# Kernel tuning notes

Measured on AMD Instinct MI355X. Metric: run time of the kernel, lower is better.

The kernel has to match this reference:

```python
import jax, jax.numpy as jnp
import numpy as np

B, T, D = 4, 4096, 1024
H, HD, K = 16, 64, 32
TAU, THRESHOLD, PULSE_BASE, N_STEPS = 0.1, 0.5, 4.0, 5


def setup_inputs() -> dict:
    key = jax.random.key(0)
    ks = jax.random.split(key, 8)
    s = 0.02
    return {
        "x": jax.random.normal(ks[0], (B, T, D), jnp.float32),
        "spectral_basis": jax.random.normal(ks[1], (B, T, K), jnp.float32) / np.sqrt(T),
        "W_qkv": jax.random.normal(ks[2], (3 * D, D), jnp.float32) * s,
        "W_out": jax.random.normal(ks[3], (D, D), jnp.float32) * s,
        "a": jnp.float32(0.7),
        "b": jnp.float32(0.8),
        "W1": jax.random.normal(ks[4], (HD // 2, HD), jnp.float32) * s,
        "b1": jnp.zeros((HD // 2,), jnp.float32),
        "W2": jax.random.normal(ks[5], (1, HD // 2), jnp.float32) * s,
        "b2": jnp.zeros((1,), jnp.float32),
        "spectral_filter": jnp.full((H, 32), 0.5, jnp.float32),
    }


def soliton_dynamics(stimulus, a, b):
    # stimulus: (B, H, K, HD); FitzHugh-Nagumo style 5-step Euler integration
    dt = 1.0 / N_STEPS
    v = jnp.zeros_like(stimulus)
    w = jnp.zeros_like(stimulus)
    stim_scale = jnp.clip(jnp.max(jnp.abs(stimulus), axis=-1, keepdims=True), 1e-06, None)
    stim_n = stimulus / stim_scale
    I = jnp.where(jnp.abs(stimulus) > THRESHOLD, stim_n, stim_n * 0.1)
    for _ in range(N_STEPS):
        dv = v - v ** 3 / 3 - w + I
        dw = (v + a - b * w) / TAU
        v = jnp.clip(v + dt * dv, -3.0, 3.0)
        w = jnp.clip(w + dt * dw, -3.0, 3.0)
    return v * stim_scale, v


def reference(x, spectral_basis, W_qkv, W_out, a, b, W1, b1, W2, b2, spectral_filter):
    Bx, Tx, Dx = x.shape
    k = spectral_basis.shape[-1]
    qkv = x @ W_qkv.T                                   # (B,T,3D)
    qkv = qkv.reshape(Bx, Tx, 3, H, HD).transpose(2, 0, 3, 1, 4)
    q, kk, v = qkv[0], qkv[1], qkv[2]                   # (B,H,T,HD)

    qm = q.mean(axis=2)                                 # (B,H,HD)
    h1 = jax.nn.silu(qm @ W1.T + b1)
    pulse_widths = PULSE_BASE + jax.nn.softplus(h1 @ W2.T + b2)[..., 0]  # (B,H)

    q_spec = jnp.einsum('bhtd,btk->bhkd', q, spectral_basis)
    k_spec = jnp.einsum('bhtd,btk->bhkd', kk, spectral_basis)
    attn_spec = jnp.einsum('bhkd,bhkd->bhk', q_spec, k_spec) / np.sqrt(HD)
    filt = jax.nn.sigmoid(spectral_filter[:, :k])       # (H,k)
    attn_spec = attn_spec * filt[None]

    stim = jnp.broadcast_to(attn_spec[..., None], (Bx, H, k, HD))
    response, state = soliton_dynamics(stim, a, b)
    response = response.mean(axis=-1)                   # (B,H,k)

    v_spec = jnp.einsum('bhtd,btk->bhkd', v, spectral_basis)
    out_spec = response[..., None] * v_spec             # (B,H,k,HD)
    out = jnp.einsum('bhkd,btk->bhtd', out_spec, spectral_basis)
    out = out.transpose(0, 2, 1, 3).reshape(Bx, Tx, Dx)
    out = out @ W_out.T
    return out, pulse_widths, response
```

## Files before the change

kernel.cpp:

```cpp
#include <hip/hip_runtime.h>

#define B_ 4
#define T_ 4096
#define D_ 1024
#define H_ 16
#define K_ 32


__global__ __launch_bounds__(256) void reduce_zp(
    const float4* __restrict__ src, float4* __restrict__ dst,
    const int n4, const int z, const int stride4, const int total4)
{
  int i = blockIdx.x * 256 + threadIdx.x;
  if (i >= total4) return;
  if (i >= n4){
    float4 zv; zv.x = 0.f; zv.y = 0.f; zv.z = 0.f; zv.w = 0.f;
    dst[i] = zv; return;
  }
  float s0 = 0.f, s1 = 0.f, s2 = 0.f, s3 = 0.f;
  const float4* p = src + i;
  for (int zz = 0; zz < z; ++zz){
    float4 v = p[(size_t)zz * stride4];
    s0 += v.x; s1 += v.y; s2 += v.z; s3 += v.w;
  }
  float4 o; o.x = s0; o.y = s1; o.z = s2; o.w = s3;
  dst[i] = o;
}

__global__ __launch_bounds__(256) void reduce_z(
    const float4* __restrict__ src, float4* __restrict__ dst,
    const int n4, const int z, const int stride4)
{
  int i = blockIdx.x * 256 + threadIdx.x;
  if (i >= n4) return;
  float s0 = 0.f, s1 = 0.f, s2 = 0.f, s3 = 0.f;
  const float4* p = src + i;
  for (int zz = 0; zz < z; ++zz){
    float4 v = p[(size_t)zz * stride4];
    s0 += v.x; s1 += v.y; s2 += v.z; s3 += v.w;
  }
  float4 o; o.x = s0; o.y = s1; o.z = s2; o.w = s3;
  dst[i] = o;
}

__global__ __launch_bounds__(256) void k1_spectral_p(
    const float* __restrict__ x, const float* __restrict__ sb,
    float* __restrict__ XP)
{
  const int b  = blockIdx.y;
  const int zz = blockIdx.z;
  const int t0 = zz * 64;
  const int c  = blockIdx.x * 256 + threadIdx.x;
  __shared__ __align__(16) float sbs[64][36];
  #pragma unroll
  for (int i = 0; i < 8; i++){
    int idx = threadIdx.x + i * 256;
    int k = idx & 31, t = idx >> 5;
    sbs[t][k] = sb[(size_t)(b * T_ + t0 + t) * K_ + k];
  }
  __syncthreads();
  float acc[32];
  #pragma unroll
  for (int k = 0; k < 32; k++) acc[k] = 0.f;
  float am = 0.f;
  const float* xp = x + (size_t)(b * T_ + t0) * D_ + c;
  float p0 = xp[0];
  float p1 = xp[D_];
  float p2 = xp[2 * D_];
  float p3 = xp[3 * D_];
  #pragma unroll 4
  for (int t = 0; t < 64; ++t){
    float xv = p0; p0 = p1; p1 = p2; p2 = p3;
    if (t < 60) p3 = xp[(size_t)(t + 4) * D_];
    am += xv;
    const float4* srow = (const float4*)&sbs[t][0];
    #pragma unroll
    for (int j = 0; j < 8; j++){
      float4 s4 = srow[j];
      acc[j * 4 + 0] = fmaf(s4.x, xv, acc[j * 4 + 0]);
      acc[j * 4 + 1] = fmaf(s4.y, xv, acc[j * 4 + 1]);
      acc[j * 4 + 2] = fmaf(s4.z, xv, acc[j * 4 + 2]);
      acc[j * 4 + 3] = fmaf(s4.w, xv, acc[j * 4 + 3]);
    }
  }
  float* o = XP + (size_t)zz * 135168 + (size_t)(b * K_) * D_ + c;
  #pragma unroll
  for (int k = 0; k < 32; k++) o[(size_t)k * D_] = acc[k];
  XP[(size_t)zz * 135168 + 131072 + b * D_ + c] = am;
}

__global__ __launch_bounds__(256) void gemm_aw_p(
    const float* __restrict__ A, const float* __restrict__ W,
    float* __restrict__ Cp, const int N, const int cPerSplit, const int MN)
{
  __shared__ __align__(16) float As[32][68];
  __shared__ __align__(16) float Ws[32][68];
  const int nt = blockIdx.x, mt = blockIdx.y;
  const int cbase = blockIdx.z * cPerSplit;
  const int tx = threadIdx.x & 15, ty = threadIdx.x >> 4;
  const int sc = threadIdx.x & 31, sr = threadIdx.x >> 5;
  float acc[4][4];
  #pragma unroll
  for (int i = 0; i < 4; i++)
    #pragma unroll
    for (int j = 0; j < 4; j++) acc[i][j] = 0.f;

  float ra[8], rw[8];
  const float* Ap = A + (size_t)(mt * 64 + sr) * 1024 + cbase + sc;
  const float* Wp = W + (size_t)(nt * 64 + sr) * 1024 + cbase + sc;
  #pragma unroll
  for (int i = 0; i < 8; i++){ ra[i] = Ap[(size_t)(i * 8) * 1024];
                               rw[i] = Wp[(size_t)(i * 8) * 1024]; }
  #pragma unroll
  for (int i = 0; i < 8; i++){ As[sc][sr + i * 8] = ra[i];
                               Ws[sc][sr + i * 8] = rw[i]; }
  __syncthreads();

  for (int cc = 32; cc < cPerSplit; cc += 32){
    #pragma unroll
    for (int i = 0; i < 8; i++){ ra[i] = Ap[(size_t)(i * 8) * 1024 + cc];
                                 rw[i] = Wp[(size_t)(i * 8) * 1024 + cc]; }
    #pragma unroll 4
    for (int c = 0; c < 32; ++c){
      const float4 a4 = *(const float4*)&As[c][ty * 4];
      const float4 w4 = *(const float4*)&Ws[c][tx * 4];
      acc[0][0] = fmaf(a4.x, w4.x, acc[0][0]);
      acc[0][1] = fmaf(a4.x, w4.y, acc[0][1]);
      acc[0][2] = fmaf(a4.x, w4.z, acc[0][2]);
      acc[0][3] = fmaf(a4.x, w4.w, acc[0][3]);
      acc[1][0] = fmaf(a4.y, w4.x, acc[1][0]);
      acc[1][1] = fmaf(a4.y, w4.y, acc[1][1]);
      acc[1][2] = fmaf(a4.y, w4.z, acc[1][2]);
      acc[1][3] = fmaf(a4.y, w4.w, acc[1][3]);
      acc[2][0] = fmaf(a4.z, w4.x, acc[2][0]);
      acc[2][1] = fmaf(a4.z, w4.y, acc[2][1]);
      acc[2][2] = fmaf(a4.z, w4.z, acc[2][2]);
      acc[2][3] = fmaf(a4.z, w4.w, acc[2][3]);
      acc[3][0] = fmaf(a4.w, w4.x, acc[3][0]);
      acc[3][1] = fmaf(a4.w, w4.y, acc[3][1]);
      acc[3][2] = fmaf(a4.w, w4.z, acc[3][2]);
      acc[3][3] = fmaf(a4.w, w4.w, acc[3][3]);
    }
    __syncthreads();
    #pragma unroll
    for (int i = 0; i < 8; i++){ As[sc][sr + i * 8] = ra[i];
                                 Ws[sc][sr + i * 8] = rw[i]; }
    __syncthreads();
  }
  #pragma unroll 4
  for (int c = 0; c < 32; ++c){
    const float4 a4 = *(const float4*)&As[c][ty * 4];
    const float4 w4 = *(const float4*)&Ws[c][tx * 4];
    acc[0][0] = fmaf(a4.x, w4.x, acc[0][0]);
    acc[0][1] = fmaf(a4.x, w4.y, acc[0][1]);
    acc[0][2] = fmaf(a4.x, w4.z, acc[0][2]);
    acc[0][3] = fmaf(a4.x, w4.w, acc[0][3]);
    acc[1][0] = fmaf(a4.y, w4.x, acc[1][0]);
    acc[1][1] = fmaf(a4.y, w4.y, acc[1][1]);
    acc[1][2] = fmaf(a4.y, w4.z, acc[1][2]);
    acc[1][3] = fmaf(a4.y, w4.w, acc[1][3]);
    acc[2][0] = fmaf(a4.z, w4.x, acc[2][0]);
    acc[2][1] = fmaf(a4.z, w4.y, acc[2][1]);
    acc[2][2] = fmaf(a4.z, w4.z, acc[2][2]);
    acc[2][3] = fmaf(a4.z, w4.w, acc[2][3]);
    acc[3][0] = fmaf(a4.w, w4.x, acc[3][0]);
    acc[3][1] = fmaf(a4.w, w4.y, acc[3][1]);
    acc[3][2] = fmaf(a4.w, w4.z, acc[3][2]);
    acc[3][3] = fmaf(a4.w, w4.w, acc[3][3]);
  }
  float* cp = Cp + (size_t)blockIdx.z * MN;
  #pragma unroll
  for (int i = 0; i < 4; i++){
    float4 o; o.x = acc[i][0]; o.y = acc[i][1]; o.z = acc[i][2]; o.w = acc[i][3];
    *(float4*)(cp + (size_t)(mt * 64 + ty * 4 + i) * N + nt * 64 + tx * 4) = o;
  }
}

__global__ __launch_bounds__(64) void k3_small(
    const float* __restrict__ qkvC,
    const float* __restrict__ W1, const float* __restrict__ b1,
    const float* __restrict__ W2, const float* __restrict__ b2,
    const float* __restrict__ filt,
    const float* __restrict__ a_in, const float* __restrict__ b_in,
    float* __restrict__ u, float* __restrict__ out_pulse,
    float* __restrict__ out_resp)
{
  const int b = blockIdx.x >> 4, h = blockIdx.x & 15;
  const int d = threadIdx.x;
  __shared__ float qm[64];
  __shared__ float h1s[32];
  __shared__ float rsp[32];
  qm[d] = qkvC[(size_t)(128 + b) * 3072 + h * 64 + d] * (1.0f / 4096.0f);
  __syncthreads();
  if (d < 32){
    float z = b1[d];
    for (int j = 0; j < 64; j++) z = fmaf(qm[j], W1[d * 64 + j], z);
    h1s[d] = z / (1.0f + __expf(-z));
  }
  __syncthreads();
  if (d == 0){
    float z2 = b2[0];
    for (int j = 0; j < 32; j++) z2 = fmaf(h1s[j], W2[j], z2);
    out_pulse[b * H_ + h] = 4.0f + log1pf(__expf(z2));
  }
  if (d < 32){
    const int k = d;
    const float* qrow = qkvC + (size_t)(b * K_ + k) * 3072 + h * 64;
    const float* krow = qrow + 1024;
    float s = 0.f;
    for (int j = 0; j < 64; j++) s = fmaf(qrow[j], krow[j], s);
    float fg = 1.0f / (1.0f + __expf(-filt[h * 32 + k]));
    s = s * 0.125f * fg;
    float av = a_in[0], bv = b_in[0];
    float sc = fmaxf(fabsf(s), 1e-6f);
    float sn = s / sc;
    float I  = (fabsf(s) > 0.5f) ? sn : 0.1f * sn;
    float v = 0.f, w = 0.f;
    #pragma unroll
    for (int it = 0; it < 5; ++it){
      float dv = v - v * v * v * (1.0f / 3.0f) - w + I;
      float dw = (v + av - bv * w) * 10.0f;
      v = fminf(fmaxf(v + 0.2f * dv, -3.0f), 3.0f);
      w = fminf(fmaxf(w + 0.2f * dw, -3.0f), 3.0f);
    }
    float r = v * sc;
    rsp[k] = r;
    out_resp[(b * H_ + h) * K_ + k] = r;
  }
  __syncthreads();
  for (int k = 0; k < 32; k++){
    u[(size_t)(b * K_ + k) * D_ + h * 64 + d] =
        rsp[k] * qkvC[(size_t)(b * K_ + k) * 3072 + 2048 + h * 64 + d];
  }
}

__global__ __launch_bounds__(256) void k4_main(
    const float* __restrict__ sb, const float* __restrict__ Mf,
    float* __restrict__ out)
{
  const int yy = blockIdx.y;
  const int r0 = (yy < 56 ? yy : yy + 8) * 16;
  const int b  = r0 >> 12;
  const int e0 = blockIdx.x * 512 + threadIdx.x * 2;
  __shared__ __align__(16) float sbs[16][36];
  #pragma unroll
  for (int i = 0; i < 2; i++){
    int idx = threadIdx.x + i * 256;
    int k = idx & 31, t = idx >> 5;
    sbs[t][k] = sb[(size_t)(r0 + t) * K_ + k];
  }
  __syncthreads();
  float mx[32], my[32];
  const float* mp = Mf + (size_t)b * K_ * D_ + e0;
  #pragma unroll
  for (int k = 0; k < 32; k++){ mx[k] = mp[(size_t)k * D_]; my[k] = mp[(size_t)k * D_ + 1]; }
  float* op = out + (size_t)r0 * D_ + e0;
  for (int t = 0; t < 16; ++t){
    float ox = 0.f, oy = 0.f;
    const float4* srow = (const float4*)&sbs[t][0];
    #pragma unroll
    for (int j = 0; j < 8; j++){
      float4 s4 = srow[j];
      ox = fmaf(s4.x, mx[j * 4 + 0], ox); oy = fmaf(s4.x, my[j * 4 + 0], oy);
      ox = fmaf(s4.y, mx[j * 4 + 1], ox); oy = fmaf(s4.y, my[j * 4 + 1], oy);
      ox = fmaf(s4.z, mx[j * 4 + 2], ox); oy = fmaf(s4.z, my[j * 4 + 2], oy);
      ox = fmaf(s4.w, mx[j * 4 + 3], ox); oy = fmaf(s4.w, my[j * 4 + 3], oy);
    }
    float2 o2; o2.x = ox; o2.y = oy;
    *(float2*)(op + (size_t)t * D_) = o2;
  }
}

__global__ __launch_bounds__(256) void k4_tailp(
    const float* __restrict__ sb, const float* __restrict__ Mf,
    float* __restrict__ out)
{
  __shared__ float sbs[128][33];
  __shared__ __align__(16) float Ms[32][16];
  const int j = blockIdx.x;
  #pragma unroll
  for (int i = 0; i < 2; i++){
    int idx = threadIdx.x + i * 256;
    int k = idx >> 4, e = idx & 15;
    Ms[k][e] = Mf[(size_t)k * D_ + j * 16 + e];
  }
  #pragma unroll
  for (int i = 0; i < 16; i++){
    int idx = threadIdx.x + i * 256;
    int k = idx & 31, t = idx >> 5;
    sbs[t][k] = sb[(size_t)(896 + t) * K_ + k];
  }
  __syncthreads();
  const int t  = threadIdx.x >> 1;
  const int c0 = (threadIdx.x & 1) * 8;
  float a0 = 0.f, a1 = 0.f, a2 = 0.f, a3 = 0.f;
  float a4 = 0.f, a5 = 0.f, a6 = 0.f, a7 = 0.f;
  #pragma unroll
  for (int k = 0; k < 32; k++){
    float s = sbs[t][k];
    const float4 m0 = *(const float4*)&Ms[k][c0];
    const float4 m1 = *(const float4*)&Ms[k][c0 + 4];
    a0 = fmaf(s, m0.x, a0); a1 = fmaf(s, m0.y, a1);
    a2 = fmaf(s, m0.z, a2); a3 = fmaf(s, m0.w, a3);
    a4 = fmaf(s, m1.x, a4); a5 = fmaf(s, m1.y, a5);
    a6 = fmaf(s, m1.z, a6); a7 = fmaf(s, m1.w, a7);
  }
  float* op = out + (size_t)(896 + t) * D_ + j * 16 + c0;
  float4 o0; o0.x = a0; o0.y = a1; o0.z = a2; o0.w = a3;
  float4 o1; o1.x = a4; o1.y = a5; o1.z = a6; o1.w = a7;
  *(float4*)(op)     = o0;
  *(float4*)(op + 4) = o1;
}

extern "C" void kernel_launch(void* const* d_in, const int* in_sizes, int n_in,
                              void* d_out, int out_size, void* d_ws, size_t ws_size,
                              hipStream_t stream)
{
  const float* x    = (const float*)d_in[0];
  const float* sb   = (const float*)d_in[1];
  const float* Wqkv = (const float*)d_in[2];
  const float* Wout = (const float*)d_in[3];
  const float* a_in = (const float*)d_in[4];
  const float* b_in = (const float*)d_in[5];
  const float* W1   = (const float*)d_in[6];
  const float* b1   = (const float*)d_in[7];
  const float* W2   = (const float*)d_in[8];
  const float* b2   = (const float*)d_in[9];
  const float* filt = (const float*)d_in[10];

  float* outF = (float*)d_out;
  float* qkv  = outF + 196608;
  float* u    = outF + 786432;
  float* Mm   = outF + 917504;
  float* S    = outF + 1048576;
  float* pulse = outF + 16777216;
  float* resp  = outF + 16777280;

  k1_spectral_p<<<dim3(4, 4, 64), 256, 0, stream>>>(x, sb, S);
  reduce_zp<<<dim3(192), 256, 0, stream>>>((const float4*)S, (float4*)outF,
                                           33792, 64, 33792, 49152);

  gemm_aw_p<<<dim3(48, 3, 16), 256, 0, stream>>>(outF, Wqkv, S, 3072, 64, 589824);
  reduce_z<<<dim3(576), 256, 0, stream>>>((const float4*)S, (float4*)qkv,
                                          147456, 16, 147456);

  k3_small<<<dim3(64), dim3(64), 0, stream>>>(qkv, W1, b1, W2, b2,
                                              filt, a_in, b_in, u,
                                              pulse, resp);

  gemm_aw_p<<<dim3(16, 2, 32), 256, 0, stream>>>(u, Wout, S, 1024, 32, 131072);
  reduce_z<<<dim3(128), 256, 0, stream>>>((const float4*)S, (float4*)Mm,
                                          32768, 32, 32768);

  k4_main<<<dim3(2, 1016), 256, 0, stream>>>(sb, Mm, outF);
  k4_tailp<<<dim3(64), 256, 0, stream>>>(sb, Mm, outF);
}
```

Measured before the change: 273.0 us.

## Vectorize spectral projection and output kernels, split reductions into two stages

The spectral projection kernel now has each thread handle four columns as float4, and the K dimension is split across blocks in halves of 16 instead of one block covering all 32 columns. The split-K partial-sum reductions become two-stage passes using a new grouped reduce kernel, so more blocks run in parallel and each does a shorter serial chain. The output kernel processes float4 per thread in a single block per row tile. This trades extra launches and scratch-buffer traffic for wider memory accesses and more parallel reduction work, and it raises register pressure from the float4 accumulators.

```diff
diff --git a/kernel.cpp b/kernel.cpp
--- a/kernel.cpp
+++ b/kernel.cpp
@@ -7,6 +7,29 @@
 #define K_ 32
 
 
+__device__ __forceinline__ void fma4(float4& a, float s, const float4& v){
+  a.x = fmaf(s, v.x, a.x); a.y = fmaf(s, v.y, a.y);
+  a.z = fmaf(s, v.z, a.z); a.w = fmaf(s, v.w, a.w);
+}
+
+__global__ __launch_bounds__(256) void reduce_g(
+    const float4* __restrict__ src, float4* __restrict__ dst,
+    const int n4, const int zper, const int stride4)
+{
+  const int g = blockIdx.y;
+  int i = blockIdx.x * 256 + threadIdx.x;
+  if (i >= n4) return;
+  float s0 = 0.f, s1 = 0.f, s2 = 0.f, s3 = 0.f;
+  const float4* p = src + (size_t)g * zper * stride4 + i;
+  #pragma unroll 4
+  for (int zz = 0; zz < zper; ++zz){
+    float4 v = p[(size_t)zz * stride4];
+    s0 += v.x; s1 += v.y; s2 += v.z; s3 += v.w;
+  }
+  float4 o; o.x = s0; o.y = s1; o.z = s2; o.w = s3;
+  dst[(size_t)g * stride4 + i] = o;
+}
+
 __global__ __launch_bounds__(256) void reduce_zp(
     const float4* __restrict__ src, float4* __restrict__ dst,
     const int n4, const int z, const int stride4, const int total4)
@@ -19,6 +42,7 @@
   }
   float s0 = 0.f, s1 = 0.f, s2 = 0.f, s3 = 0.f;
   const float4* p = src + i;
+  #pragma unroll 4
   for (int zz = 0; zz < z; ++zz){
     float4 v = p[(size_t)zz * stride4];
     s0 += v.x; s1 += v.y; s2 += v.z; s3 += v.w;
@@ -35,6 +59,7 @@
   if (i >= n4) return;
   float s0 = 0.f, s1 = 0.f, s2 = 0.f, s3 = 0.f;
   const float4* p = src + i;
+  #pragma unroll 4
   for (int zz = 0; zz < z; ++zz){
     float4 v = p[(size_t)zz * stride4];
     s0 += v.x; s1 += v.y; s2 += v.z; s3 += v.w;
@@ -47,46 +72,49 @@
     const float* __restrict__ x, const float* __restrict__ sb,
     float* __restrict__ XP)
 {
+  const int kh = blockIdx.x;
   const int b  = blockIdx.y;
   const int zz = blockIdx.z;
   const int t0 = zz * 64;
-  const int c  = blockIdx.x * 256 + threadIdx.x;
-  __shared__ __align__(16) float sbs[64][36];
-  #pragma unroll
-  for (int i = 0; i < 8; i++){
+  const int c  = threadIdx.x * 4;
+  __shared__ __align__(16) float sbs[64][20];
+  #pragma unroll
+  for (int i = 0; i < 4; i++){
     int idx = threadIdx.x + i * 256;
-    int k = idx & 31, t = idx >> 5;
-    sbs[t][k] = sb[(size_t)(b * T_ + t0 + t) * K_ + k];
-  }
-  __syncthreads();
-  float acc[32];
-  #pragma unroll
-  for (int k = 0; k < 32; k++) acc[k] = 0.f;
-  float am = 0.f;
+    int t = idx >> 4, kk = idx & 15;
+    sbs[t][kk] = sb[(size_t)(b * T_ + t0 + t) * K_ + kh * 16 + kk];
+  }
+  __syncthreads();
+  float4 acc[16];
+  #pragma unroll
+  for (int k = 0; k < 16; k++){ acc[k].x = 0.f; acc[k].y = 0.f;
+                                acc[k].z = 0.f; acc[k].w = 0.f; }
+  float4 am; am.x = 0.f; am.y = 0.f; am.z = 0.f; am.w = 0.f;
   const float* xp = x + (size_t)(b * T_ + t0) * D_ + c;
-  float p0 = xp[0];
-  float p1 = xp[D_];
-  float p2 = xp[2 * D_];
-  float p3 = xp[3 * D_];
+  float4 p0 = *(const float4*)(xp);
+  float4 p1 = *(const float4*)(xp + D_);
+  float4 p2 = *(const float4*)(xp + 2 * D_);
+  float4 p3 = *(const float4*)(xp + 3 * D_);
   #pragma unroll 4
   for (int t = 0; t < 64; ++t){
-    float xv = p0; p0 = p1; p1 = p2; p2 = p3;
-    if (t < 60) p3 = xp[(size_t)(t + 4) * D_];
-    am += xv;
+    float4 xv = p0; p0 = p1; p1 = p2; p2 = p3;
+    if (t < 60) p3 = *(const float4*)(xp + (size_t)(t + 4) * D_);
+    if (kh == 0){ am.x += xv.x; am.y += xv.y; am.z += xv.z; am.w += xv.w; }
     const float4* srow = (const float4*)&sbs[t][0];
     #pragma unroll
-    for (int j = 0; j < 8; j++){
+    for (int j = 0; j < 4; j++){
       float4 s4 = srow[j];
-      acc[j * 4 + 0] = fmaf(s4.x, xv, acc[j * 4 + 0]);
-      acc[j * 4 + 1] = fmaf(s4.y, xv, acc[j * 4 + 1]);
-      acc[j * 4 + 2] = fmaf(s4.z, xv, acc[j * 4 + 2]);
-      acc[j * 4 + 3] = fmaf(s4.w, xv, acc[j * 4 + 3]);
+      fma4(acc[j * 4 + 0], s4.x, xv);
+      fma4(acc[j * 4 + 1], s4.y, xv);
+      fma4(acc[j * 4 + 2], s4.z, xv);
+      fma4(acc[j * 4 + 3], s4.w, xv);
     }
   }
-  float* o = XP + (size_t)zz * 135168 + (size_t)(b * K_) * D_ + c;
-  #pragma unroll
-  for (int k = 0; k < 32; k++) o[(size_t)k * D_] = acc[k];
-  XP[(size_t)zz * 135168 + 131072 + b * D_ + c] = am;
+  float* o = XP + (size_t)zz * 135168 + (size_t)(b * K_ + kh * 16) * D_ + c;
+  #pragma unroll
+  for (int k = 0; k < 16; k++) *(float4*)(o + (size_t)k * D_) = acc[k];
+  if (kh == 0)
+    *(float4*)(XP + (size_t)zz * 135168 + 131072 + b * D_ + c) = am;
 }
 
 __global__ __launch_bounds__(256) void gemm_aw_p(
@@ -238,10 +266,10 @@
     const float* __restrict__ sb, const float* __restrict__ Mf,
     float* __restrict__ out)
 {
-  const int yy = blockIdx.y;
+  const int yy = blockIdx.x;
   const int r0 = (yy < 56 ? yy : yy + 8) * 16;
   const int b  = r0 >> 12;
-  const int e0 = blockIdx.x * 512 + threadIdx.x * 2;
+  const int e0 = threadIdx.x * 4;
   __shared__ __align__(16) float sbs[16][36];
   #pragma unroll
   for (int i = 0; i < 2; i++){
@@ -250,24 +278,24 @@
     sbs[t][k] = sb[(size_t)(r0 + t) * K_ + k];
   }
   __syncthreads();
-  float mx[32], my[32];
+  float4 m4[32];
   const float* mp = Mf + (size_t)b * K_ * D_ + e0;
   #pragma unroll
-  for (int k = 0; k < 32; k++){ mx[k] = mp[(size_t)k * D_]; my[k] = mp[(size_t)k * D_ + 1]; }
+  for (int k = 0; k < 32; k++) m4[k] = *(const float4*)(mp + (size_t)k * D_);
   float* op = out + (size_t)r0 * D_ + e0;
+  #pragma unroll 4
   for (int t = 0; t < 16; ++t){
-    float ox = 0.f, oy = 0.f;
+    float4 o4; o4.x = 0.f; o4.y = 0.f; o4.z = 0.f; o4.w = 0.f;
     const float4* srow = (const float4*)&sbs[t][0];
     #pragma unroll
     for (int j = 0; j < 8; j++){
       float4 s4 = srow[j];
-      ox = fmaf(s4.x, mx[j * 4 + 0], ox); oy = fmaf(s4.x, my[j * 4 + 0], oy);
-      ox = fmaf(s4.y, mx[j * 4 + 1], ox); oy = fmaf(s4.y, my[j * 4 + 1], oy);
-      ox = fmaf(s4.z, mx[j * 4 + 2], ox); oy = fmaf(s4.z, my[j * 4 + 2], oy);
-      ox = fmaf(s4.w, mx[j * 4 + 3], ox); oy = fmaf(s4.w, my[j * 4 + 3], oy);
+      fma4(o4, s4.x, m4[j * 4 + 0]);
+      fma4(o4, s4.y, m4[j * 4 + 1]);
+      fma4(o4, s4.z, m4[j * 4 + 2]);
+      fma4(o4, s4.w, m4[j * 4 + 3]);
     }
-    float2 o2; o2.x = ox; o2.y = oy;
-    *(float2*)(op + (size_t)t * D_) = o2;
+    *(float4*)(op + (size_t)t * D_) = o4;
   }
 }
 
@@ -333,12 +361,16 @@
   float* u    = outF + 786432;
   float* Mm   = outF + 917504;
   float* S    = outF + 1048576;
+  float* S2   = outF + 9699328;
+  float* S3   = outF + 5242880;
   float* pulse = outF + 16777216;
   float* resp  = outF + 16777280;
 
-  k1_spectral_p<<<dim3(4, 4, 64), 256, 0, stream>>>(x, sb, S);
-  reduce_zp<<<dim3(192), 256, 0, stream>>>((const float4*)S, (float4*)outF,
-                                           33792, 64, 33792, 49152);
+  k1_spectral_p<<<dim3(2, 4, 64), 256, 0, stream>>>(x, sb, S);
+  reduce_g<<<dim3(132, 8), 256, 0, stream>>>((const float4*)S, (float4*)S2,
+                                             33792, 8, 33792);
+  reduce_zp<<<dim3(192), 256, 0, stream>>>((const float4*)S2, (float4*)outF,
+                                           33792, 8, 33792, 49152);
 
   gemm_aw_p<<<dim3(48, 3, 16), 256, 0, stream>>>(outF, Wqkv, S, 3072, 64, 589824);
   reduce_z<<<dim3(576), 256, 0, stream>>>((const float4*)S, (float4*)qkv,
@@ -349,9 +381,11 @@
                                               pulse, resp);
 
   gemm_aw_p<<<dim3(16, 2, 32), 256, 0, stream>>>(u, Wout, S, 1024, 32, 131072);
-  reduce_z<<<dim3(128), 256, 0, stream>>>((const float4*)S, (float4*)Mm,
-                                          32768, 32, 32768);
-
-  k4_main<<<dim3(2, 1016), 256, 0, stream>>>(sb, Mm, outF);
+  reduce_g<<<dim3(128, 8), 256, 0, stream>>>((const float4*)S, (float4*)S3,
+                                             32768, 4, 32768);
+  reduce_z<<<dim3(128), 256, 0, stream>>>((const float4*)S3, (float4*)Mm,
+                                          32768, 8, 32768);
+
+  k4_main<<<dim3(1016), 256, 0, stream>>>(sb, Mm, outF);
   k4_tailp<<<dim3(64), 256, 0, stream>>>(sb, Mm, outF);
 }
```

New measurement: 280.0 us. 1.03x slower.
